# Optimization experiments

Measured on AMD Instinct MI355X. Metric: run time of the kernel, lower is better.

Reference implementation:

```python
import jax, jax.numpy as jnp
import numpy as np

C = 256
CK = C // 8  # qk projection dim


def setup_inputs() -> dict:
    key = jax.random.key(0)
    ks = jax.random.split(key, 8)
    B, H, W = 4, 64, 64
    x = jax.random.normal(ks[0], (B, C, W, H), dtype=jnp.float32)
    s = 1.0 / np.sqrt(C)
    Wf = jax.random.normal(ks[1], (CK, C), dtype=jnp.float32) * s
    bf = jax.random.normal(ks[2], (CK,), dtype=jnp.float32) * 0.01
    Wg = jax.random.normal(ks[3], (CK, C), dtype=jnp.float32) * s
    bg = jax.random.normal(ks[4], (CK,), dtype=jnp.float32) * 0.01
    Wh = jax.random.normal(ks[5], (C, C), dtype=jnp.float32) * s
    bh = jax.random.normal(ks[6], (C,), dtype=jnp.float32) * 0.01
    gamma = jax.random.normal(ks[7], (1,), dtype=jnp.float32) * 0.1
    return {"x": x, "Wf": Wf, "bf": bf, "Wg": Wg, "bg": bg,
            "Wh": Wh, "bh": bh, "gamma": gamma}


def reference(x, Wf, bf, Wg, bg, Wh, bh, gamma):
    B, Cc, Wd, Hd = x.shape
    N = Wd * Hd
    xf = x.reshape(B, Cc, N)  # B C N
    # 1x1 conv1d == channel matmul
    f = jnp.einsum('oc,bcn->bon', Wf, xf) + bf[None, :, None]  # B CK N
    g = jnp.einsum('oc,bcn->bon', Wg, xf) + bg[None, :, None]  # B CK N
    h = jnp.einsum('oc,bcn->bon', Wh, xf) + bh[None, :, None]  # B C N
    # s[b,i,j] = sum_k f[b,k,i] g[b,k,j]
    s = jnp.einsum('bki,bkj->bij', f, g)  # B N N
    attention = jax.nn.softmax(s, axis=-1)
    # out[b,c,i] = sum_j h[b,c,j] attention[b,i,j]
    out = jnp.einsum('bcj,bij->bci', h, attention)  # B C N
    out = out.reshape(B, Cc, Wd, Hd)
    return gamma[0] * out + x
```

## Files before the change

kernel.cpp:

```cpp
#include <hip/hip_runtime.h>

typedef __bf16 bf16x8 __attribute__((ext_vector_type(8)));
typedef __bf16 bf16x4 __attribute__((ext_vector_type(4)));
typedef float f32x4 __attribute__((ext_vector_type(4)));
typedef float f32x16 __attribute__((ext_vector_type(16)));

__device__ __forceinline__ f32x4 mfma16(bf16x8 a, bf16x8 b, f32x4 c) {
  return __builtin_amdgcn_mfma_f32_16x16x32_bf16(a, b, c, 0, 0, 0);
}
__device__ __forceinline__ f32x16 mfma32(bf16x8 a, bf16x8 b, f32x16 c) {
  return __builtin_amdgcn_mfma_f32_32x32x16_bf16(a, b, c, 0, 0, 0);
}

__device__ __forceinline__ unsigned int cvtpk(float a, float b) {
  union { __bf16 h[2]; unsigned int u; } r;
  r.h[0] = (__bf16)a; r.h[1] = (__bf16)b;
  return r.u;
}
__device__ __forceinline__ void swap32(unsigned int &a, unsigned int &b) {
  asm("v_permlane32_swap_b32 %0, %1" : "+v"(a), "+v"(b));
}

__device__ __forceinline__ void sync_lds() {
  asm volatile("s_waitcnt lgkmcnt(0)" ::: "memory");
  __builtin_amdgcn_s_barrier();
}

__global__ void wcvt_kernel(const float* __restrict__ Wf, const float* __restrict__ Wg,
                            const float* __restrict__ Wh, __bf16* __restrict__ Wb) {
  int i = blockIdx.x * 256 + threadIdx.x;
  float v;
  if (i < 8192)       v = Wf[i];
  else if (i < 16384) v = Wg[i - 8192];
  else                v = Wh[i - 16384];
  Wb[i] = (__bf16)v;
}

__global__ __launch_bounds__(512) void proj_kernel(
    const float* __restrict__ x, const float* __restrict__ bfv,
    const float* __restrict__ bgv, const float* __restrict__ bhv,
    const __bf16* __restrict__ Wb, __bf16* __restrict__ qkpk,
    __bf16* __restrict__ vpk) {
  __shared__ __align__(16) char smem[2560 + 18432];
  __bf16* xT = (__bf16*)smem;
  __bf16* ho = (__bf16*)(smem + 2560);

  const int t = threadIdx.x;
  const int l = t & 63, wg = t >> 6, q = l >> 4, l15 = l & 15;
  const int nh = wg & 1, oh = wg >> 1;
  const int bi = blockIdx.x;
  const int b = bi >> 7;
  const int nt = bi & 127;
  const int n0 = nt << 5;

  const float* xb = x + (size_t)b * 256 * 4096;

  f32x4 acc[5];
#pragma unroll
  for (int i = 0; i < 5; i++) acc[i] = (f32x4){0.f, 0.f, 0.f, 0.f};

  const int c_rel = t >> 4;
  const int n2 = (t & 15) * 2;

#pragma unroll 1
  for (int kc = 0; kc < 8; kc++) {
    __syncthreads();
    float2 v = *(const float2*)(xb + (size_t)(kc * 32 + c_rel) * 4096 + n0 + n2);
    xT[(n2 + 0) * 40 + c_rel] = (__bf16)v.x;
    xT[(n2 + 1) * 40 + c_rel] = (__bf16)v.y;
    __syncthreads();
    bf16x8 af = *(const bf16x8*)(xT + (nh * 16 + l15) * 40 + q * 8);
    const __bf16* wp = Wb + (size_t)(oh * 80 + l15) * 256 + kc * 32 + q * 8;
#pragma unroll
    for (int ot = 0; ot < 5; ot++) {
      bf16x8 bfr = *(const bf16x8*)(wp + (size_t)ot * 16 * 256);
      acc[ot] = mfma16(af, bfr, acc[ot]);
    }
  }

#pragma unroll
  for (int ot = 0; ot < 5; ot++) {
    int o = oh * 80 + ot * 16 + l15;
    float bias = (o < 32) ? bfv[o] : (o < 64) ? bgv[o - 32] : bhv[o - 64];
    if (oh == 0 && ot < 4) {
      int qk = o >> 5, fr = (o >> 4) & 1, hh = (o >> 3) & 1, e = o & 7;
      size_t base = ((size_t)b * 128 + nt) * 2048 + qk * 1024 + fr * 512 + hh * 256;
#pragma unroll
      for (int r = 0; r < 4; r++) {
        int n_rel = nh * 16 + q * 4 + r;
        qkpk[base + n_rel * 8 + e] = (__bf16)(acc[ot][r] + bias);
      }
    } else {
#pragma unroll
      for (int r = 0; r < 4; r++) {
        int n_rel = nh * 16 + q * 4 + r;
        ho[(o - 64) * 36 + n_rel] = (__bf16)(acc[ot][r] + bias);
      }
    }
  }
  __syncthreads();
  unsigned short* vpku = (unsigned short*)vpk + (size_t)b * 1048576;
  const unsigned short* hou = (const unsigned short*)ho;
  for (int e = t; e < 4096; e += 512) {
    int c = e >> 4, nn = (e & 15) * 2;
    int n = n0 + nn;
    int jc = n >> 4, hh = (n >> 3) & 1, ee = n & 7;
    unsigned int vv = *(const unsigned int*)(hou + c * 36 + nn);
    *(unsigned int*)(vpku + (((size_t)(jc * 2 + hh) * 256 + c) * 8 + ee)) = vv;
  }
}

__global__ __launch_bounds__(512, 2) void attn_kernel(
    const __bf16* __restrict__ qkpk, const __bf16* __restrict__ vpk,
    __bf16* __restrict__ pO, float* __restrict__ Lp) {
  __shared__ __align__(16) char smem[139264];
  __bf16* Vbuf = (__bf16*)smem;

  const int t = threadIdx.x;
  const int l = t & 63, w = t >> 6;
  const int h = l >> 5, l31 = l & 31;

  const int bi = blockIdx.x;
  const int xcd = bi & 7;
  const int combo = xcd * 2 + ((bi >> 3) & 1);
  const int ig = bi >> 4;
  const int b = combo >> 2, jp = combo & 3;
  const int ti = ig * 8 + w;
  const int n0 = ti << 5;

  const __bf16* qkb = qkpk + (size_t)b * 262144;
  const __bf16* vpb = vpk + (size_t)b * 1048576;
  const int jq0 = jp << 10;

  const __bf16* qp = qkb + (size_t)ti * 2048 + h * 256 + l31 * 8;
  const bf16x8 qf0 = *(const bf16x8*)(qp);
  const bf16x8 qf1 = *(const bf16x8*)(qp + 512);

  f32x16 acc[8] = {};
  float rsum = 0.f;

  const __bf16* kbase = qkb + 1024 + h * 256 + l31 * 8;
  const int vfo = h * 2048 + l31 * 8;

  bf16x8 kf0 = *(const bf16x8*)(kbase + (size_t)(jq0 >> 5) * 2048);
  bf16x8 kf1 = *(const bf16x8*)(kbase + (size_t)(jq0 >> 5) * 2048 + 512);

  {
    const __bf16* src = vpb + (size_t)(jq0 >> 4) * 4096;
    bf16x8 a = *(const bf16x8*)(src + t * 8);
    bf16x8 c = *(const bf16x8*)(src + 4096 + t * 8);
    *(bf16x8*)(Vbuf + t * 8) = a;
    *(bf16x8*)(Vbuf + 4096 + t * 8) = c;
  }
  sync_lds();

#pragma unroll 1
  for (int ch = 0; ch < 32; ++ch) {
    bf16x8 sv0, sv1;
    if (ch < 31) {
      const __bf16* src = vpb + (size_t)((jq0 >> 4) + (ch + 1) * 2) * 4096;
      sv0 = *(const bf16x8*)(src + t * 8);
      sv1 = *(const bf16x8*)(src + 4096 + t * 8);
    }

    f32x16 s = {};
    s = mfma32(kf0, qf0, s);
    s = mfma32(kf1, qf1, s);

    if (ch < 31) {
      const __bf16* kp = kbase + (size_t)((jq0 >> 5) + ch + 1) * 2048;
      kf0 = *(const bf16x8*)(kp);
      kf1 = *(const bf16x8*)(kp + 512);
    }

    float p[16];
#pragma unroll
    for (int r = 0; r < 16; r++) { p[r] = __expf(s[r]); rsum += p[r]; }

    unsigned int u0 = cvtpk(p[0], p[1]), v0 = cvtpk(p[2], p[3]);
    unsigned int w0 = cvtpk(p[4], p[5]), z0 = cvtpk(p[6], p[7]);
    swap32(u0, w0); swap32(v0, z0);
    unsigned int u1 = cvtpk(p[8], p[9]), v1 = cvtpk(p[10], p[11]);
    unsigned int w1 = cvtpk(p[12], p[13]), z1 = cvtpk(p[14], p[15]);
    swap32(u1, w1); swap32(v1, z1);
    union { unsigned int u[4]; bf16x8 v; } A0, A1;
    A0.u[0] = u0; A0.u[1] = v0; A0.u[2] = w0; A0.u[3] = z0;
    A1.u[0] = u1; A1.u[1] = v1; A1.u[2] = w1; A1.u[3] = z1;

    const __bf16* rb = Vbuf + (ch & 1) * 8192;
#pragma unroll
    for (int ct = 0; ct < 8; ct++) {
      bf16x8 vv = *(const bf16x8*)(rb + vfo + ct * 256);
      acc[ct] = mfma32(A0.v, vv, acc[ct]);
    }
#pragma unroll
    for (int ct = 0; ct < 8; ct++) {
      bf16x8 vv = *(const bf16x8*)(rb + 4096 + vfo + ct * 256);
      acc[ct] = mfma32(A1.v, vv, acc[ct]);
    }

    if (ch < 31) {
      __bf16* wb = Vbuf + ((ch + 1) & 1) * 8192;
      *(bf16x8*)(wb + t * 8) = sv0;
      *(bf16x8*)(wb + 4096 + t * 8) = sv1;
    }
    sync_lds();
  }

  __bf16* stage = (__bf16*)smem + (size_t)w * 8704;
#pragma unroll
  for (int ct = 0; ct < 8; ct++) {
    int c0 = ct * 32 + l31;
#pragma unroll
    for (int r = 0; r < 16; r++) {
      int i_loc = (r & 3) + 8 * (r >> 2) + 4 * h;
      stage[c0 * 34 + i_loc] = (__bf16)acc[ct][r];
    }
  }
  asm volatile("s_waitcnt lgkmcnt(0)" ::: "memory");

  unsigned short* ob = (unsigned short*)pO + (size_t)(jp * 4 + b) * 1048576 + n0;
  const unsigned short* su = (const unsigned short*)stage;
#pragma unroll 1
  for (int e = l; e < 4096; e += 64) {
    int c = e >> 4, i2 = (e & 15) * 2;
    unsigned int vv = *(const unsigned int*)(su + c * 34 + i2);
    *(unsigned int*)(ob + (size_t)c * 4096 + i2) = vv;
  }

  rsum += __shfl_xor(rsum, 32);
  if (l < 32) Lp[(size_t)(jp * 4 + b) * 4096 + n0 + l] = rsum;
}

__global__ __launch_bounds__(256) void norm_kernel(
    const float* __restrict__ x, const float* __restrict__ gamma_p,
    const __bf16* __restrict__ pO, const float* __restrict__ Lp,
    float* __restrict__ out) {
  const int bc = blockIdx.x;
  const int b = bc >> 8;
  const float gm = gamma_p[0];
  const float* xr = x + (size_t)bc * 4096;
  float* orow = out + (size_t)bc * 4096;
  const __bf16* pbase = pO + (size_t)bc * 4096;
  const float* lbase = Lp + (size_t)b * 4096;

  for (int i0 = threadIdx.x * 4; i0 < 4096; i0 += 1024) {
    float4 xv = *(const float4*)(xr + i0);
    float s0 = 0.f, s1 = 0.f, s2 = 0.f, s3 = 0.f;
    float l0 = 0.f, l1 = 0.f, l2 = 0.f, l3 = 0.f;
#pragma unroll
    for (int jp = 0; jp < 4; jp++) {
      bf16x4 pv = *(const bf16x4*)(pbase + (size_t)jp * 4194304 + i0);
      s0 += (float)pv[0]; s1 += (float)pv[1]; s2 += (float)pv[2]; s3 += (float)pv[3];
      float4 lv = *(const float4*)(lbase + (size_t)jp * 16384 + i0);
      l0 += lv.x; l1 += lv.y; l2 += lv.z; l3 += lv.w;
    }
    float4 ov;
    ov.x = gm * s0 / l0 + xv.x;
    ov.y = gm * s1 / l1 + xv.y;
    ov.z = gm * s2 / l2 + xv.z;
    ov.w = gm * s3 / l3 + xv.w;
    *(float4*)(orow + i0) = ov;
  }
}

extern "C" void kernel_launch(void* const* d_in, const int* in_sizes, int n_in,
                              void* d_out, int out_size, void* d_ws, size_t ws_size,
                              hipStream_t stream) {
  const float* x   = (const float*)d_in[0];
  const float* Wf  = (const float*)d_in[1];
  const float* bfv = (const float*)d_in[2];
  const float* Wg  = (const float*)d_in[3];
  const float* bgv = (const float*)d_in[4];
  const float* Wh  = (const float*)d_in[5];
  const float* bhv = (const float*)d_in[6];
  const float* gm  = (const float*)d_in[7];
  float* out = (float*)d_out;

  char* ws = (char*)d_ws;
  __bf16* Wb   = (__bf16*)ws;
  __bf16* qkpk = (__bf16*)(ws + 262144);
  __bf16* vpk  = (__bf16*)(ws + 2359296);
  __bf16* pO   = (__bf16*)(ws + 10747904);
  float*  Lp   = (float*)(ws + 44302336);

  hipLaunchKernelGGL(wcvt_kernel, dim3(320), dim3(256), 0, stream, Wf, Wg, Wh, Wb);
  hipLaunchKernelGGL(proj_kernel, dim3(512), dim3(512), 0, stream,
                     x, bfv, bgv, bhv, Wb, qkpk, vpk);
  hipLaunchKernelGGL(attn_kernel, dim3(256), dim3(512), 0, stream,
                     qkpk, vpk, pO, Lp);
  hipLaunchKernelGGL(norm_kernel, dim3(1024), dim3(256), 0, stream,
                     x, gm, pO, Lp, out);
}
```

Before: 161.0 us.

## Software-pipeline QK scores and softmax packing one tile ahead of PV MFMAs

Restructures the attention loop so the score MFMAs and exp/pack for tile ch+1 run while the PV MFMAs for tile ch are issuing, with the key loads prefetched two tiles ahead. The goal is to hide the exp and permute latency behind matrix-core work. It also folds log2(e) into the stored key projection so the loop can use exp2f in place of __expf. The cost is extra live registers (next-tile scores and packed fragments), which could raise register pressure.

```diff
diff --git a/kernel.cpp b/kernel.cpp
--- a/kernel.cpp
+++ b/kernel.cpp
@@ -24,6 +24,23 @@
 __device__ __forceinline__ void sync_lds() {
   asm volatile("s_waitcnt lgkmcnt(0)" ::: "memory");
   __builtin_amdgcn_s_barrier();
+}
+
+__device__ __forceinline__ void pack_tile(const f32x16 s, float &rs,
+                                          bf16x8 &A0v, bf16x8 &A1v) {
+  float p[16];
+#pragma unroll
+  for (int r = 0; r < 16; r++) { p[r] = exp2f(s[r]); rs += p[r]; }
+  unsigned int a0 = cvtpk(p[0], p[1]), a1 = cvtpk(p[2], p[3]);
+  unsigned int a2 = cvtpk(p[4], p[5]), a3 = cvtpk(p[6], p[7]);
+  swap32(a0, a2); swap32(a1, a3);
+  unsigned int a4 = cvtpk(p[8], p[9]), a5 = cvtpk(p[10], p[11]);
+  unsigned int a6 = cvtpk(p[12], p[13]), a7 = cvtpk(p[14], p[15]);
+  swap32(a4, a6); swap32(a5, a7);
+  union { unsigned int u[4]; bf16x8 v; } A0, A1;
+  A0.u[0] = a0; A0.u[1] = a1; A0.u[2] = a2; A0.u[3] = a3;
+  A1.u[0] = a4; A1.u[1] = a5; A1.u[2] = a6; A1.u[3] = a7;
+  A0v = A0.v; A1v = A1.v;
 }
 
 __global__ void wcvt_kernel(const float* __restrict__ Wf, const float* __restrict__ Wg,
@@ -85,10 +102,11 @@
     if (oh == 0 && ot < 4) {
       int qk = o >> 5, fr = (o >> 4) & 1, hh = (o >> 3) & 1, e = o & 7;
       size_t base = ((size_t)b * 128 + nt) * 2048 + qk * 1024 + fr * 512 + hh * 256;
+      float sc = (o >= 32) ? 1.44269504089f : 1.0f;
 #pragma unroll
       for (int r = 0; r < 4; r++) {
         int n_rel = nh * 16 + q * 4 + r;
-        qkpk[base + n_rel * 8 + e] = (__bf16)(acc[ot][r] + bias);
+        qkpk[base + n_rel * 8 + e] = (__bf16)((acc[ot][r] + bias) * sc);
       }
     } else {
 #pragma unroll
@@ -142,16 +160,24 @@
   const __bf16* kbase = qkb + 1024 + h * 256 + l31 * 8;
   const int vfo = h * 2048 + l31 * 8;
 
-  bf16x8 kf0 = *(const bf16x8*)(kbase + (size_t)(jq0 >> 5) * 2048);
-  bf16x8 kf1 = *(const bf16x8*)(kbase + (size_t)(jq0 >> 5) * 2048 + 512);
-
+  bf16x8 pac0, pac1;
   {
     const __bf16* src = vpb + (size_t)(jq0 >> 4) * 4096;
-    bf16x8 a = *(const bf16x8*)(src + t * 8);
-    bf16x8 c = *(const bf16x8*)(src + 4096 + t * 8);
-    *(bf16x8*)(Vbuf + t * 8) = a;
-    *(bf16x8*)(Vbuf + 4096 + t * 8) = c;
-  }
+    bf16x8 sa = *(const bf16x8*)(src + t * 8);
+    bf16x8 sc = *(const bf16x8*)(src + 4096 + t * 8);
+
+    bf16x8 k0 = *(const bf16x8*)(kbase + (size_t)(jq0 >> 5) * 2048);
+    bf16x8 k1 = *(const bf16x8*)(kbase + (size_t)(jq0 >> 5) * 2048 + 512);
+    f32x16 s = {};
+    s = mfma32(k0, qf0, s);
+    s = mfma32(k1, qf1, s);
+    pack_tile(s, rsum, pac0, pac1);
+
+    *(bf16x8*)(Vbuf + t * 8) = sa;
+    *(bf16x8*)(Vbuf + 4096 + t * 8) = sc;
+  }
+  bf16x8 kf0 = *(const bf16x8*)(kbase + (size_t)((jq0 >> 5) + 1) * 2048);
+  bf16x8 kf1 = *(const bf16x8*)(kbase + (size_t)((jq0 >> 5) + 1) * 2048 + 512);
   sync_lds();
 
 #pragma unroll 1
@@ -163,43 +189,36 @@
       sv1 = *(const bf16x8*)(src + 4096 + t * 8);
     }
 
-    f32x16 s = {};
-    s = mfma32(kf0, qf0, s);
-    s = mfma32(kf1, qf1, s);
-
+    f32x16 s_next = {};
     if (ch < 31) {
-      const __bf16* kp = kbase + (size_t)((jq0 >> 5) + ch + 1) * 2048;
+      s_next = mfma32(kf0, qf0, s_next);
+      s_next = mfma32(kf1, qf1, s_next);
+    }
+    if (ch < 30) {
+      const __bf16* kp = kbase + (size_t)((jq0 >> 5) + ch + 2) * 2048;
       kf0 = *(const bf16x8*)(kp);
       kf1 = *(const bf16x8*)(kp + 512);
     }
 
-    float p[16];
-#pragma unroll
-    for (int r = 0; r < 16; r++) { p[r] = __expf(s[r]); rsum += p[r]; }
-
-    unsigned int u0 = cvtpk(p[0], p[1]), v0 = cvtpk(p[2], p[3]);
-    unsigned int w0 = cvtpk(p[4], p[5]), z0 = cvtpk(p[6], p[7]);
-    swap32(u0, w0); swap32(v0, z0);
-    unsigned int u1 = cvtpk(p[8], p[9]), v1 = cvtpk(p[10], p[11]);
-    unsigned int w1 = cvtpk(p[12], p[13]), z1 = cvtpk(p[14], p[15]);
-    swap32(u1, w1); swap32(v1, z1);
-    union { unsigned int u[4]; bf16x8 v; } A0, A1;
-    A0.u[0] = u0; A0.u[1] = v0; A0.u[2] = w0; A0.u[3] = z0;
-    A1.u[0] = u1; A1.u[1] = v1; A1.u[2] = w1; A1.u[3] = z1;
-
     const __bf16* rb = Vbuf + (ch & 1) * 8192;
+
 #pragma unroll
     for (int ct = 0; ct < 8; ct++) {
       bf16x8 vv = *(const bf16x8*)(rb + vfo + ct * 256);
-      acc[ct] = mfma32(A0.v, vv, acc[ct]);
-    }
+      acc[ct] = mfma32(pac0, vv, acc[ct]);
+    }
+
+    bf16x8 pan0, pan1;
+    if (ch < 31) pack_tile(s_next, rsum, pan0, pan1);
+
 #pragma unroll
     for (int ct = 0; ct < 8; ct++) {
       bf16x8 vv = *(const bf16x8*)(rb + 4096 + vfo + ct * 256);
-      acc[ct] = mfma32(A1.v, vv, acc[ct]);
+      acc[ct] = mfma32(pac1, vv, acc[ct]);
     }
 
     if (ch < 31) {
+      pac0 = pan0; pac1 = pan1;
       __bf16* wb = Vbuf + ((ch + 1) & 1) * 8192;
       *(bf16x8*)(wb + t * 8) = sv0;
       *(bf16x8*)(wb + 4096 + t * 8) = sv1;
```

After: 170.4 us. +5.8%, slower.
